# Kernel optimization log

Hardware: AMD Instinct MI355X
Metric: run time of the kernel (lower is better)

Reference implementation:

```python
import jax, jax.numpy as jnp
import numpy as np


def setup_inputs() -> dict:
    key = jax.random.key(0)
    k_y, k_cb = jax.random.split(key)
    B, C, H, W = 8, 192, 64, 64
    G, K = 8, 512
    d = C // G  # 24
    y = jax.random.normal(k_y, (B, C, H, W), dtype=jnp.float32)
    codebooks = jax.random.normal(k_cb, (G, K, d), dtype=jnp.float32)
    return {"y": y, "codebooks": codebooks}


def reference(y, codebooks):
    # y: [B, C, H, W]; codebooks: [G, K, d] with C == G*d
    B, C, H, W = y.shape
    G, K, d = codebooks.shape
    # split channels into G groups of dim d -> vectors at each spatial pos
    x = y.reshape(B, G, d, H, W).transpose(0, 3, 4, 1, 2)  # [B,H,W,G,d]
    x2 = jnp.sum(x * x, axis=-1, keepdims=True)            # [B,H,W,G,1]
    e2 = jnp.sum(codebooks * codebooks, axis=-1)           # [G,K]
    xe = jnp.einsum('bhwgd,gkd->bhwgk', x, codebooks)      # [B,H,W,G,K]
    dist = x2 - 2.0 * xe + e2                              # [B,H,W,G,K]
    idx = jnp.argmin(dist, axis=-1)                        # [B,H,W,G] int
    # gather quantized vectors per group (to_feather)
    q = codebooks[jnp.arange(G), idx]                      # [B,H,W,G,d]
    y_ba = q.transpose(0, 3, 4, 1, 2).reshape(B, C, H, W)  # [B,C,H,W]
    code_index = idx.transpose(0, 3, 1, 2)                 # [B,G,H,W]
    # straight-through estimator
    universal_ctx = y + jax.lax.stop_gradient(y_ba - y)
    return universal_ctx, y_ba, code_index[:, None]        # [B,1,G,H,W]
```

## Files before the change

kernel.cpp:

```cpp
#include <hip/hip_runtime.h>

#define B_   8
#define C_   192
#define HW_  4096
#define G_   8
#define K_   512
#define D_   24
#define CBSZ (K_ * D_)
#define THREADS 512
#define NBLOCKS 1024

#define FRAG_HW   12288
#define IMG_HW    13312
#define TILES_PER_GROUP 2048
#define WAVES_PER_GROUP 1024

typedef float  f32x4 __attribute__((ext_vector_type(4)));
typedef int    i32x4 __attribute__((ext_vector_type(4)));
typedef short  s16x8 __attribute__((ext_vector_type(8)));
typedef short  s16x4 __attribute__((ext_vector_type(4)));
typedef unsigned long long u64;

static __device__ __forceinline__ unsigned umin_(unsigned a, unsigned b){return a<b?a:b;}
static __device__ __forceinline__ unsigned umax_(unsigned a, unsigned b){return a>b?a:b;}
static __device__ __forceinline__ unsigned short f2bf(float x){
    unsigned u=__float_as_uint(x);
    return (unsigned short)((u + 0x7FFFu + ((u>>16)&1u))>>16);
}

__global__ __launch_bounds__(THREADS, 8) void vq_mfma7(
    const float* __restrict__ y, const float* __restrict__ cb,
    float* __restrict__ out)
{
    __shared__ __align__(16) unsigned short sB[IMG_HW];

    const int bid = blockIdx.x;
    const int g = bid & 7;
    const int blkg = bid >> 3;
    const int tid = threadIdx.x;
    const int wave = tid >> 6, lane = tid & 63;
    const int c = lane & 15, q = lane >> 4;

    const float* cbg = cb + g * CBSZ;

    #pragma unroll
    for (int it = 0; it < 6; ++it) {
        int gi = it * THREADS + tid;
        f32x4 v = ((const f32x4*)cbg)[gi];
        int i4 = gi << 2;
        int n  = i4 / 24;
        int k0 = i4 - n * 24;
        int off = (n >> 4) * 384 + (((k0 >> 3) << 4) + (n & 15)) * 8 + (k0 & 7);
        s16x4 h;
        h[0]=(short)f2bf(v[0]); h[1]=(short)f2bf(v[1]);
        h[2]=(short)f2bf(v[2]); h[3]=(short)f2bf(v[3]);
        *(s16x4*)(&sB[off]) = h;
    }
    {
        const int n = tid;
        const float* row = cbg + n * D_;
        double s0 = 0.0, s1 = 0.0;
        #pragma unroll
        for (int j = 0; j < D_; j += 2) {
            double v0 = (double)row[j], v1 = (double)row[j+1];
            s0 = fma(v0,v0,s0); s1 = fma(v1,v1,s1);
        }
        ((float*)(sB + FRAG_HW))[n] = (float)(256.0 + s0 + s1);
    }
    __syncthreads();

    float* out0 = out;
    float* out1 = out + B_*C_*HW_;
    float* out2 = out + 2*B_*C_*HW_;

    const unsigned short* aptr = sB + (lane < 48 ? lane : lane - 48) * 8;
    const f32x4* e2p = (const f32x4*)((const float*)(sB + FRAG_HW) + (q << 2));

    const int wsid = (blkg << 3) + wave;

    for (int tt = wsid; tt < TILES_PER_GROUP; tt += WAVES_PER_GROUP) {
        const int bimg = tt >> 8;
        const int hw   = (tt & 255) << 4;
        const int ybase = (bimg*C_ + g*D_)*HW_ + hw;
        const float* yb = y + ybase;

        float xf[8];
        unsigned hx[4], lx[4];
        if (q < 3) {
            const float* yq = yb + (q*8)*HW_ + c;
            #pragma unroll
            for (int jj = 0; jj < 8; ++jj) xf[jj] = -2.0f * yq[jj*HW_];
            #pragma unroll
            for (int p2 = 0; p2 < 4; ++p2) {
                float f0 = xf[2*p2], f1 = xf[2*p2+1];
                unsigned u0 = __float_as_uint(f0), u1v = __float_as_uint(f1);
                hx[p2] = (u1v & 0xFFFF0000u) | (u0 >> 16);
                float l0 = f0 - __uint_as_float(u0 & 0xFFFF0000u);
                float l1 = f1 - __uint_as_float(u1v & 0xFFFF0000u);
                lx[p2] = (unsigned)f2bf(l0) | ((unsigned)f2bf(l1) << 16);
            }
        } else {
            #pragma unroll
            for (int jj = 0; jj < 8; ++jj) xf[jj] = 0.0f;
            hx[0]=0u; hx[1]=0u; hx[2]=0u; hx[3]=0u;
            lx[0]=0u; lx[1]=0u; lx[2]=0u; lx[3]=0u;
        }
        const s16x8 Xh = __builtin_bit_cast(s16x8, (i32x4){(int)hx[0],(int)hx[1],(int)hx[2],(int)hx[3]});
        const s16x8 Xl = __builtin_bit_cast(s16x8, (i32x4){(int)lx[0],(int)lx[1],(int)lx[2],(int)lx[3]});

        unsigned b1=0xFFFFFFFFu, b2=0xFFFFFFFFu, b3=0xFFFFFFFFu;
        const unsigned qr4 = (unsigned)(q << 2);
        #pragma unroll 8
        for (int t = 0; t < 32; ++t) {
            s16x8 eh = *(const s16x8*)(aptr + t * 384);
            f32x4 acc = e2p[t * 4];
            acc = __builtin_amdgcn_mfma_f32_16x16x32_bf16(eh, Xh, acc, 0,0,0);
            acc = __builtin_amdgcn_mfma_f32_16x16x32_bf16(eh, Xl, acc, 0,0,0);
            const unsigned cbase = ((unsigned)t << 4) + qr4;
            #pragma unroll
            for (int r = 0; r < 4; ++r) {
                unsigned key = (__float_as_uint(acc[r]) & 0xFFFFFE00u) + (cbase + r);
                unsigned t3, t2;
                asm("v_med3_u32 %0, %1, %2, %3" : "=v"(t3) : "v"(key), "v"(b2), "v"(b3));
                asm("v_med3_u32 %0, %1, %2, %3" : "=v"(t2) : "v"(key), "v"(b1), "v"(b2));
                b3 = t3; b2 = t2;
                b1 = umin_(b1, key);
            }
        }

        #pragma unroll
        for (int d = 16; d < 64; d <<= 1) {
            unsigned o1=__shfl_xor(b1,d,64), o2=__shfl_xor(b2,d,64), o3=__shfl_xor(b3,d,64);
            unsigned x = umax_(b1,o1);
            unsigned yv= umin_(b2,o2);
            unsigned w = umax_(b2,o2);
            unsigned z = umin_(b3,o3);
            b1 = umin_(b1,o1);
            b2 = umin_(x,yv);
            b3 = umin_(umax_(x,yv), umin_(w,z));
        }

        const float v1 = __uint_as_float(b1 & 0xFFFFFE00u);
        const float v2 = __uint_as_float(b2 & 0xFFFFFE00u);
        int kwin;
        if (__ballot((v2 - v1) < 0.20f) == 0ull) {
            kwin = (int)(b1 & 511u);
        } else {
            double xd[8];
            #pragma unroll
            for (int jj = 0; jj < 8; ++jj) xd[jj] = (double)xf[jj];
            const unsigned cands[3] = {b1, b2, b3};
            u64 bestk = ~0ull;
            #pragma unroll
            for (int ci = 0; ci < 3; ++ci) {
                int kc = (int)(cands[ci] & 511u);
                double s = 0.0;
                if (q < 3) {
                    const f32x4* ce4 = (const f32x4*)(cbg + kc*D_ + (q<<3));
                    float ef[8];
                    *(f32x4*)&ef[0] = ce4[0];
                    *(f32x4*)&ef[4] = ce4[1];
                    #pragma unroll
                    for (int jj = 0; jj < 8; ++jj) {
                        double ev = (double)ef[jj];
                        s = fma(ev, ev, s);
                        s = fma(xd[jj], ev, s);
                    }
                }
                s += __shfl_xor(s, 16, 64);
                s += __shfl_xor(s, 32, 64);
                s += 256.0;
                u64 kk = (((u64)__double_as_longlong(s)) & ~0x1FFull) | (u64)kc;
                bestk = kk < bestk ? kk : bestk;
            }
            kwin = (int)(bestk & 511ull);
        }

        const float* cw = cbg + kwin * D_;
        if (q < 3) {
            const f32x4* cw4 = (const f32x4*)(cw + (q<<3));
            float v[8];
            *(f32x4*)&v[0] = cw4[0];
            *(f32x4*)&v[4] = cw4[1];
            const int ob = ybase + (q*8)*HW_ + c;
            #pragma unroll
            for (int jj = 0; jj < 8; ++jj) {
                out0[ob + jj*HW_] = v[jj];
                out1[ob + jj*HW_] = v[jj];
            }
        }
        if (lane < 16)
            out2[(bimg*G_ + g)*HW_ + hw + lane] = (float)kwin;
    }
}

extern "C" void kernel_launch(void* const* d_in, const int* in_sizes, int n_in,
                              void* d_out, int out_size, void* d_ws, size_t ws_size,
                              hipStream_t stream) {
    const float* y  = (const float*)d_in[0];
    const float* cb = (const float*)d_in[1];
    float* out = (float*)d_out;
    (void)d_ws; (void)ws_size;

    vq_mfma7<<<dim3(NBLOCKS), dim3(THREADS), 0, stream>>>(y, cb, out);
}
```

Baseline: 112.7 us.

## Process both tiles per wave together to share codebook fragment loads

Each wave now handles its two tiles in a single pass through the codebook. Each LDS codebook fragment and e2 load feeds four MFMAs instead of two, and the two independent accumulator chains give more instruction-level parallelism. The codebook staging is rewritten so each thread converts one full row, which reuses the loaded values for the norm and avoids reading the codebook twice. The tiebreak path now reloads y from global memory instead of keeping xf live, which cuts register pressure but adds loads when that rare path runs.

Measured after the change: 115.3 us. 1.02x slower.

```diff
diff --git a/kernel.cpp b/kernel.cpp
--- a/kernel.cpp
+++ b/kernel.cpp
@@ -12,8 +12,6 @@
 
 #define FRAG_HW   12288
 #define IMG_HW    13312
-#define TILES_PER_GROUP 2048
-#define WAVES_PER_GROUP 1024
 
 typedef float  f32x4 __attribute__((ext_vector_type(4)));
 typedef int    i32x4 __attribute__((ext_vector_type(4)));
@@ -28,7 +26,7 @@
     return (unsigned short)((u + 0x7FFFu + ((u>>16)&1u))>>16);
 }
 
-__global__ __launch_bounds__(THREADS, 8) void vq_mfma7(
+__global__ __launch_bounds__(THREADS, 8) void vq_mfma8(
     const float* __restrict__ y, const float* __restrict__ cb,
     float* __restrict__ out)
 {
@@ -43,27 +41,29 @@
 
     const float* cbg = cb + g * CBSZ;
 
-    #pragma unroll
-    for (int it = 0; it < 6; ++it) {
-        int gi = it * THREADS + tid;
-        f32x4 v = ((const f32x4*)cbg)[gi];
-        int i4 = gi << 2;
-        int n  = i4 / 24;
-        int k0 = i4 - n * 24;
-        int off = (n >> 4) * 384 + (((k0 >> 3) << 4) + (n & 15)) * 8 + (k0 & 7);
-        s16x4 h;
-        h[0]=(short)f2bf(v[0]); h[1]=(short)f2bf(v[1]);
-        h[2]=(short)f2bf(v[2]); h[3]=(short)f2bf(v[3]);
-        *(s16x4*)(&sB[off]) = h;
-    }
     {
         const int n = tid;
-        const float* row = cbg + n * D_;
+        const f32x4* row4 = (const f32x4*)(cbg + n * D_);
+        f32x4 rr[6];
+        #pragma unroll
+        for (int kb = 0; kb < 6; ++kb) rr[kb] = row4[kb];
+        const int nb = (n >> 4) * 384 + (n & 15) * 8;
+        #pragma unroll
+        for (int kb = 0; kb < 6; ++kb) {
+            const int k0 = kb * 4;
+            const int off = nb + ((k0 >> 3) << 7) + (k0 & 7);
+            s16x4 h;
+            h[0]=(short)f2bf(rr[kb][0]); h[1]=(short)f2bf(rr[kb][1]);
+            h[2]=(short)f2bf(rr[kb][2]); h[3]=(short)f2bf(rr[kb][3]);
+            *(s16x4*)(&sB[off]) = h;
+        }
         double s0 = 0.0, s1 = 0.0;
         #pragma unroll
-        for (int j = 0; j < D_; j += 2) {
-            double v0 = (double)row[j], v1 = (double)row[j+1];
+        for (int kb = 0; kb < 6; ++kb) {
+            double v0=(double)rr[kb][0], v1=(double)rr[kb][1];
+            double v2=(double)rr[kb][2], v3=(double)rr[kb][3];
             s0 = fma(v0,v0,s0); s1 = fma(v1,v1,s1);
+            s0 = fma(v2,v2,s0); s1 = fma(v3,v3,s1);
         }
         ((float*)(sB + FRAG_HW))[n] = (float)(256.0 + s0 + s1);
     }
@@ -75,19 +75,22 @@
 
     const unsigned short* aptr = sB + (lane < 48 ? lane : lane - 48) * 8;
     const f32x4* e2p = (const f32x4*)((const float*)(sB + FRAG_HW) + (q << 2));
-
-    const int wsid = (blkg << 3) + wave;
-
-    for (int tt = wsid; tt < TILES_PER_GROUP; tt += WAVES_PER_GROUP) {
-        const int bimg = tt >> 8;
-        const int hw   = (tt & 255) << 4;
-        const int ybase = (bimg*C_ + g*D_)*HW_ + hw;
-        const float* yb = y + ybase;
-
-        float xf[8];
+    const unsigned qr4 = (unsigned)(q << 2);
+
+    const int wsid  = (blkg << 3) + wave;
+    const int hw    = (wsid & 255) << 4;
+    const int bimg0 = wsid >> 8;
+    int ybase[2];
+    ybase[0] = (bimg0*C_ + g*D_)*HW_ + hw;
+    ybase[1] = ybase[0] + 4*C_*HW_;
+
+    s16x8 Xh[2], Xl[2];
+    #pragma unroll
+    for (int ti = 0; ti < 2; ++ti) {
         unsigned hx[4], lx[4];
         if (q < 3) {
-            const float* yq = yb + (q*8)*HW_ + c;
+            const float* yq = y + ybase[ti] + (q*8)*HW_ + c;
+            float xf[8];
             #pragma unroll
             for (int jj = 0; jj < 8; ++jj) xf[jj] = -2.0f * yq[jj*HW_];
             #pragma unroll
@@ -100,34 +103,51 @@
                 lx[p2] = (unsigned)f2bf(l0) | ((unsigned)f2bf(l1) << 16);
             }
         } else {
-            #pragma unroll
-            for (int jj = 0; jj < 8; ++jj) xf[jj] = 0.0f;
             hx[0]=0u; hx[1]=0u; hx[2]=0u; hx[3]=0u;
             lx[0]=0u; lx[1]=0u; lx[2]=0u; lx[3]=0u;
         }
-        const s16x8 Xh = __builtin_bit_cast(s16x8, (i32x4){(int)hx[0],(int)hx[1],(int)hx[2],(int)hx[3]});
-        const s16x8 Xl = __builtin_bit_cast(s16x8, (i32x4){(int)lx[0],(int)lx[1],(int)lx[2],(int)lx[3]});
-
-        unsigned b1=0xFFFFFFFFu, b2=0xFFFFFFFFu, b3=0xFFFFFFFFu;
-        const unsigned qr4 = (unsigned)(q << 2);
-        #pragma unroll 8
-        for (int t = 0; t < 32; ++t) {
-            s16x8 eh = *(const s16x8*)(aptr + t * 384);
-            f32x4 acc = e2p[t * 4];
-            acc = __builtin_amdgcn_mfma_f32_16x16x32_bf16(eh, Xh, acc, 0,0,0);
-            acc = __builtin_amdgcn_mfma_f32_16x16x32_bf16(eh, Xl, acc, 0,0,0);
-            const unsigned cbase = ((unsigned)t << 4) + qr4;
-            #pragma unroll
-            for (int r = 0; r < 4; ++r) {
-                unsigned key = (__float_as_uint(acc[r]) & 0xFFFFFE00u) + (cbase + r);
+        Xh[ti] = __builtin_bit_cast(s16x8, (i32x4){(int)hx[0],(int)hx[1],(int)hx[2],(int)hx[3]});
+        Xl[ti] = __builtin_bit_cast(s16x8, (i32x4){(int)lx[0],(int)lx[1],(int)lx[2],(int)lx[3]});
+    }
+
+    unsigned b1a[2] = {0xFFFFFFFFu, 0xFFFFFFFFu};
+    unsigned b2a[2] = {0xFFFFFFFFu, 0xFFFFFFFFu};
+    unsigned b3a[2] = {0xFFFFFFFFu, 0xFFFFFFFFu};
+    #pragma unroll 4
+    for (int t = 0; t < 32; ++t) {
+        s16x8 eh  = *(const s16x8*)(aptr + t * 384);
+        f32x4 e2v = e2p[t * 4];
+        f32x4 a0 = __builtin_amdgcn_mfma_f32_16x16x32_bf16(eh, Xh[0], e2v, 0,0,0);
+        a0       = __builtin_amdgcn_mfma_f32_16x16x32_bf16(eh, Xl[0], a0,  0,0,0);
+        f32x4 a1 = __builtin_amdgcn_mfma_f32_16x16x32_bf16(eh, Xh[1], e2v, 0,0,0);
+        a1       = __builtin_amdgcn_mfma_f32_16x16x32_bf16(eh, Xl[1], a1,  0,0,0);
+        #pragma unroll
+        for (int r = 0; r < 4; ++r) {
+            const unsigned idtr = (unsigned)((t << 4) | r);
+            {
+                unsigned key = (__float_as_uint(a0[r]) & 0xFFFFFE00u) + idtr;
                 unsigned t3, t2;
-                asm("v_med3_u32 %0, %1, %2, %3" : "=v"(t3) : "v"(key), "v"(b2), "v"(b3));
-                asm("v_med3_u32 %0, %1, %2, %3" : "=v"(t2) : "v"(key), "v"(b1), "v"(b2));
-                b3 = t3; b2 = t2;
-                b1 = umin_(b1, key);
-            }
-        }
-
+                asm("v_med3_u32 %0, %1, %2, %3" : "=v"(t3) : "v"(key), "v"(b2a[0]), "v"(b3a[0]));
+                asm("v_med3_u32 %0, %1, %2, %3" : "=v"(t2) : "v"(key), "v"(b1a[0]), "v"(b2a[0]));
+                b3a[0] = t3; b2a[0] = t2; b1a[0] = umin_(b1a[0], key);
+            }
+            {
+                unsigned key = (__float_as_uint(a1[r]) & 0xFFFFFE00u) + idtr;
+                unsigned t3, t2;
+                asm("v_med3_u32 %0, %1, %2, %3" : "=v"(t3) : "v"(key), "v"(b2a[1]), "v"(b3a[1]));
+                asm("v_med3_u32 %0, %1, %2, %3" : "=v"(t2) : "v"(key), "v"(b1a[1]), "v"(b2a[1]));
+                b3a[1] = t3; b2a[1] = t2; b1a[1] = umin_(b1a[1], key);
+            }
+        }
+    }
+    #pragma unroll
+    for (int ti = 0; ti < 2; ++ti) {
+        b1a[ti] += qr4; b2a[ti] += qr4; b3a[ti] += qr4;
+    }
+
+    #pragma unroll
+    for (int ti = 0; ti < 2; ++ti) {
+        unsigned b1 = b1a[ti], b2 = b2a[ti], b3 = b3a[ti];
         #pragma unroll
         for (int d = 16; d < 64; d <<= 1) {
             unsigned o1=__shfl_xor(b1,d,64), o2=__shfl_xor(b2,d,64), o3=__shfl_xor(b3,d,64);
@@ -146,9 +166,18 @@
         if (__ballot((v2 - v1) < 0.20f) == 0ull) {
             kwin = (int)(b1 & 511u);
         } else {
+            float xfr[8];
+            if (q < 3) {
+                const float* yq = y + ybase[ti] + (q*8)*HW_ + c;
+                #pragma unroll
+                for (int jj = 0; jj < 8; ++jj) xfr[jj] = -2.0f * yq[jj*HW_];
+            } else {
+                #pragma unroll
+                for (int jj = 0; jj < 8; ++jj) xfr[jj] = 0.0f;
+            }
             double xd[8];
             #pragma unroll
-            for (int jj = 0; jj < 8; ++jj) xd[jj] = (double)xf[jj];
+            for (int jj = 0; jj < 8; ++jj) xd[jj] = (double)xfr[jj];
             const unsigned cands[3] = {b1, b2, b3};
             u64 bestk = ~0ull;
             #pragma unroll
@@ -182,15 +211,17 @@
             float v[8];
             *(f32x4*)&v[0] = cw4[0];
             *(f32x4*)&v[4] = cw4[1];
-            const int ob = ybase + (q*8)*HW_ + c;
+            const int ob = ybase[ti] + (q*8)*HW_ + c;
             #pragma unroll
             for (int jj = 0; jj < 8; ++jj) {
                 out0[ob + jj*HW_] = v[jj];
                 out1[ob + jj*HW_] = v[jj];
             }
         }
-        if (lane < 16)
+        if (lane < 16) {
+            const int bimg = bimg0 + ti*4;
             out2[(bimg*G_ + g)*HW_ + hw + lane] = (float)kwin;
+        }
     }
 }
 
@@ -202,5 +233,5 @@
     float* out = (float*)d_out;
     (void)d_ws; (void)ws_size;
 
-    vq_mfma7<<<dim3(NBLOCKS), dim3(THREADS), 0, stream>>>(y, cb, out);
+    vq_mfma8<<<dim3(NBLOCKS), dim3(THREADS), 0, stream>>>(y, cb, out);
 }
```
